# Optimization experiments

Hardware: AMD Instinct MI355X
Metric: run time of the kernel (lower is better)

Reference implementation:

```python
import jax, jax.numpy as jnp
import numpy as np

D = 2048
H = 16
HD = D // H
FF = 4 * D
EPS = 1e-5


def layernorm(x, scale, shift):
    mean = jnp.mean(x, axis=-1, keepdims=True)
    var = jnp.mean((x - mean) ** 2, axis=-1, keepdims=True)  # unbiased=False
    return scale * (x - mean) / jnp.sqrt(var + EPS) + shift


def setup_inputs() -> dict:
    key = jax.random.key(0)
    ks = jax.random.split(key, 12)
    s = 0.02
    return {
        "x": jax.random.normal(ks[0], (2, 2048, D), dtype=jnp.float32),
        "ln1_scale": jnp.ones((D,), jnp.float32),
        "ln1_shift": jnp.zeros((D,), jnp.float32),
        "wq": jax.random.normal(ks[1], (D, D), jnp.float32) * s,
        "bq": jnp.zeros((D,), jnp.float32),
        "wk": jax.random.normal(ks[2], (D, D), jnp.float32) * s,
        "bk": jnp.zeros((D,), jnp.float32),
        "wv": jax.random.normal(ks[3], (D, D), jnp.float32) * s,
        "bv": jnp.zeros((D,), jnp.float32),
        "wo": jax.random.normal(ks[4], (D, D), jnp.float32) * s,
        "bo": jnp.zeros((D,), jnp.float32),
        "ln2_scale": jnp.ones((D,), jnp.float32),
        "ln2_shift": jnp.zeros((D,), jnp.float32),
        "w1": jax.random.normal(ks[5], (D, FF), jnp.float32) * s,
        "b1": jnp.zeros((FF,), jnp.float32),
        "w2": jax.random.normal(ks[6], (FF, D), jnp.float32) * s,
        "b2": jnp.zeros((D,), jnp.float32),
    }


def block(x, ln1_scale, ln1_shift, wq, bq, wk, bk, wv, bv, wo, bo,
          ln2_scale, ln2_shift, w1, b1, w2, b2):
    B, S, _ = x.shape
    h = layernorm(x, ln1_scale, ln1_shift)
    q = (h @ wq + bq).reshape(B, S, H, HD).transpose(0, 2, 1, 3)  # [B,H,S,hd]
    k = (h @ wk + bk).reshape(B, S, H, HD).transpose(0, 2, 1, 3)
    v = (h @ wv + bv).reshape(B, S, H, HD).transpose(0, 2, 1, 3)
    scores = jnp.einsum("bhqd,bhkd->bhqk", q, k) / jnp.sqrt(jnp.float32(HD))
    causal = jnp.tril(jnp.ones((S, S), dtype=bool))
    scores = jnp.where(causal[None, None], scores, -jnp.inf)
    attn = jax.nn.softmax(scores, axis=-1)
    ctx = jnp.einsum("bhqk,bhkd->bhqd", attn, v)
    ctx = ctx.transpose(0, 2, 1, 3).reshape(B, S, D)
    x = x + (ctx @ wo + bo)
    h2 = layernorm(x, ln2_scale, ln2_shift)
    ffn = jax.nn.gelu(h2 @ w1 + b1, approximate=False) @ w2 + b2
    return x + ffn


def reference(x, ln1_scale, ln1_shift, wq, bq, wk, bk, wv, bv, wo, bo,
              ln2_scale, ln2_shift, w1, b1, w2, b2):
    return block(x, ln1_scale, ln1_shift, wq, bq, wk, bk, wv, bv, wo, bo,
                 ln2_scale, ln2_shift, w1, b1, w2, b2)
```

## Files before the change

kernel.cpp:

```cpp
#include <hip/hip_runtime.h>
#include <hip/hip_bf16.h>
#include <math.h>

namespace {

constexpr int Dm  = 2048;
constexpr int FFm = 8192;
constexpr int SEQ = 2048;
constexpr int HDm = 128;
constexpr int MR  = 4096;
constexpr int QW  = 3 * Dm;

typedef __bf16 bf16_t;
typedef __bf16 bf16x8 __attribute__((ext_vector_type(8)));
typedef float  f32x4  __attribute__((ext_vector_type(4)));

typedef __attribute__((address_space(1))) const void as1_void;
typedef __attribute__((address_space(3))) void as3_void;

__device__ __forceinline__ void gload_lds16(const void* g, void* l) {
  __builtin_amdgcn_global_load_lds((as1_void*)g, (as3_void*)l, 16, 0, 0);
}

__global__ __launch_bounds__(256)
void ln_kernel(const float* __restrict__ x, const float* __restrict__ sc,
               const float* __restrict__ sh, bf16_t* __restrict__ out)
{
  const int row = blockIdx.x;
  const int tid = threadIdx.x;
  const float4* xr = (const float4*)(x + (size_t)row * Dm);
  float4 v0 = xr[tid*2], v1 = xr[tid*2+1];
  float s  = v0.x+v0.y+v0.z+v0.w + v1.x+v1.y+v1.z+v1.w;
  float s2 = v0.x*v0.x+v0.y*v0.y+v0.z*v0.z+v0.w*v0.w
           + v1.x*v1.x+v1.y*v1.y+v1.z*v1.z+v1.w*v1.w;
  #pragma unroll
  for (int off = 32; off; off >>= 1) { s += __shfl_xor(s, off); s2 += __shfl_xor(s2, off); }
  __shared__ float red[8];
  if ((tid & 63) == 0) { red[(tid>>6)*2] = s; red[(tid>>6)*2+1] = s2; }
  __syncthreads();
  s  = red[0]+red[2]+red[4]+red[6];
  s2 = red[1]+red[3]+red[5]+red[7];
  const float mean = s * (1.f/Dm);
  const float var  = fmaxf(s2 * (1.f/Dm) - mean*mean, 0.f);
  const float rstd = rsqrtf(var + 1e-5f);
  const float4* scp = (const float4*)sc;
  const float4* shp = (const float4*)sh;
  float4 sc0 = scp[tid*2], sc1 = scp[tid*2+1];
  float4 sh0 = shp[tid*2], sh1 = shp[tid*2+1];
  __attribute__((aligned(16))) bf16_t ob[8];
  ob[0] = (bf16_t)((v0.x-mean)*rstd*sc0.x + sh0.x);
  ob[1] = (bf16_t)((v0.y-mean)*rstd*sc0.y + sh0.y);
  ob[2] = (bf16_t)((v0.z-mean)*rstd*sc0.z + sh0.z);
  ob[3] = (bf16_t)((v0.w-mean)*rstd*sc0.w + sh0.w);
  ob[4] = (bf16_t)((v1.x-mean)*rstd*sc1.x + sh1.x);
  ob[5] = (bf16_t)((v1.y-mean)*rstd*sc1.y + sh1.y);
  ob[6] = (bf16_t)((v1.z-mean)*rstd*sc1.z + sh1.z);
  ob[7] = (bf16_t)((v1.w-mean)*rstd*sc1.w + sh1.w);
  *(uint4*)(out + (size_t)row*Dm + tid*8) = *(const uint4*)ob;
}

__global__ __launch_bounds__(256)
void wconv_t(const float* __restrict__ W, bf16_t* __restrict__ WT, int K, int N)
{
  __shared__ float tile[32][33];
  const int tx = threadIdx.x & 31, ty = threadIdx.x >> 5;
  const int nb = blockIdx.x * 32, kb = blockIdx.y * 32;
  #pragma unroll
  for (int p = 0; p < 4; ++p)
    tile[ty+8*p][tx] = W[(size_t)(kb+ty+8*p)*N + nb + tx];
  __syncthreads();
  #pragma unroll
  for (int p = 0; p < 4; ++p)
    WT[(size_t)(nb+ty+8*p)*K + kb + tx] = (bf16_t)tile[tx][ty+8*p];
}

__global__ void bias_concat(const float* __restrict__ bq, const float* __restrict__ bk,
                            const float* __restrict__ bv, float* __restrict__ o)
{
  int i = blockIdx.x*256 + threadIdx.x;
  o[i] = bq[i]; o[Dm+i] = bk[i]; o[2*Dm+i] = bv[i];
}

__global__ __launch_bounds__(256)
void vtrans(const bf16_t* __restrict__ qkv, bf16_t* __restrict__ vT)
{
  __shared__ bf16_t tile[32][33];
  const int tx = threadIdx.x & 31, ty = threadIdx.x >> 5;
  const int s0 = blockIdx.x*32, d0 = blockIdx.y*32, bh = blockIdx.z;
  const int b = bh >> 4, h = bh & 15;
  const bf16_t* src = qkv + (size_t)(b*SEQ)*QW + 2*Dm + h*HDm;
  #pragma unroll
  for (int p = 0; p < 4; ++p)
    tile[ty+8*p][tx] = src[(size_t)(s0+ty+8*p)*QW + d0 + tx];
  __syncthreads();
  bf16_t* dst = vT + (size_t)bh*HDm*SEQ;
  #pragma unroll
  for (int p = 0; p < 4; ++p)
    dst[(size_t)(d0+ty+8*p)*SEQ + s0 + tx] = tile[tx][ty+8*p];
}

template<int MODE>
__global__ __launch_bounds__(512, 2)
void gemm8p(const bf16_t* __restrict__ A, const bf16_t* __restrict__ BT,
            const float* __restrict__ bias, const float* __restrict__ resid,
            void* __restrict__ Cout, void* __restrict__ Cout2,
            int Ndim, int Kslice, int Kstride, int gx)
{
  const int nwg = gridDim.x;
  int flat = blockIdx.x;
  flat = (flat & 7) * (nwg >> 3) + (flat >> 3);
  const int n0 = (flat % gx) * 256;
  const int m0 = (flat / gx) * 256;
  const int kOff = blockIdx.y * Kslice;
  const int tid = threadIdx.x;
  const int lane = tid & 63;
  const int w = tid >> 6;
  const int wr = w >> 2, wc = w & 3;
  const int lr = lane & 15, kg = lane >> 4;

  __shared__ __attribute__((aligned(16))) bf16_t lds[65536];

  f32x4 acc[8][4] = {};

  auto stageA = [&](int buf, int half, int kt) {
    const bf16_t* src = A + (size_t)(m0 + half*128)*Kstride + kOff + kt*64;
    bf16_t* dst = lds + ((buf*2+0)*2+half)*8192;
    #pragma unroll
    for (int i = 0; i < 2; ++i) {
      const int s = tid + i*512;
      const int row = s >> 3, blk = (s & 7) ^ (row & 7);
      gload_lds16(src + (size_t)row*Kstride + blk*8, dst + s*8);
    }
  };
  auto stageB = [&](int buf, int half, int kt) {
    const bf16_t* src = BT + (size_t)(n0 + half*128)*Kstride + kOff + kt*64;
    bf16_t* dst = lds + ((buf*2+1)*2+half)*8192;
    #pragma unroll
    for (int i = 0; i < 2; ++i) {
      const int s = tid + i*512;
      const int row = s >> 3, blk = (s & 7) ^ (row & 7);
      gload_lds16(src + (size_t)row*Kstride + blk*8, dst + s*8);
    }
  };
  auto readA = [&](int buf, int mh, bf16x8* f) {
    const bf16_t* base = lds + ((buf*2+0)*2+wr)*8192;
    #pragma unroll
    for (int ml = 0; ml < 4; ++ml)
      #pragma unroll
      for (int kk = 0; kk < 2; ++kk) {
        const int row = mh*64 + ml*16 + lr;
        f[ml*2+kk] = *(const bf16x8*)(base + row*64 + (((kk*4+kg) ^ (row&7))*8));
      }
  };
  auto readB = [&](int buf, int nh, bf16x8* f) {
    const bf16_t* base = lds + ((buf*2+1)*2+(wc>>1))*8192;
    #pragma unroll
    for (int nl = 0; nl < 2; ++nl)
      #pragma unroll
      for (int kk = 0; kk < 2; ++kk) {
        const int row = (wc&1)*64 + nh*32 + nl*16 + lr;
        f[nl*2+kk] = *(const bf16x8*)(base + row*64 + (((kk*4+kg) ^ (row&7))*8));
      }
  };
  auto mfma16 = [&](int mh, int nh, const bf16x8* Af, const bf16x8* Bf) {
    __builtin_amdgcn_s_setprio(1);
    #pragma unroll
    for (int ml = 0; ml < 4; ++ml)
      #pragma unroll
      for (int nl = 0; nl < 2; ++nl)
        #pragma unroll
        for (int kk = 0; kk < 2; ++kk)
          acc[mh*4+ml][nh*2+nl] =
            __builtin_amdgcn_mfma_f32_16x16x32_bf16(Af[ml*2+kk], Bf[nl*2+kk],
                                                    acc[mh*4+ml][nh*2+nl], 0, 0, 0);
    __builtin_amdgcn_s_setprio(0);
  };

#define PHASE_MID() do { __builtin_amdgcn_s_barrier(); \
    asm volatile("s_waitcnt lgkmcnt(0)" ::: "memory"); \
    __builtin_amdgcn_sched_barrier(0); } while (0)
#define PHASE_END() __builtin_amdgcn_s_barrier()
#define KGUARD(more_) do { if (more_) asm volatile("s_waitcnt vmcnt(4)" ::: "memory"); \
    else asm volatile("s_waitcnt vmcnt(0)" ::: "memory"); \
    __builtin_amdgcn_s_barrier(); } while (0)

  stageA(0,0,0); stageA(0,1,0); stageB(0,0,0); stageB(0,1,0);
  stageA(1,0,1); stageA(1,1,1);
  asm volatile("s_waitcnt vmcnt(4)" ::: "memory");
  __builtin_amdgcn_s_barrier();

  const int NITER = Kslice >> 7;
  for (int j = 0; j < NITER; ++j) {
    const int t0 = 2*j, t1 = 2*j + 1;
    const bool more = (j + 1 < NITER);
    bf16x8 Af0[8], Af1[8], Bf0[4], Bf1[4];

    readA(0,0,Af0); readB(0,0,Bf0);
    stageB(1,0,t1);
    PHASE_MID(); mfma16(0,0,Af0,Bf0); PHASE_END();
    readA(0,1,Af1);
    stageB(1,1,t1);
    PHASE_MID(); mfma16(1,0,Af1,Bf0); PHASE_END();
    readB(0,1,Bf1);
    if (more) stageA(0,0,t0+2);
    PHASE_MID(); mfma16(1,1,Af1,Bf1); PHASE_END();
    if (more) stageA(0,1,t0+2);
    PHASE_MID(); mfma16(0,1,Af0,Bf1);
    KGUARD(more);

    readA(1,0,Af0); readB(1,0,Bf0);
    if (more) stageB(0,0,t0+2);
    PHASE_MID(); mfma16(0,0,Af0,Bf0); PHASE_END();
    readA(1,1,Af1);
    if (more) stageB(0,1,t0+2);
    PHASE_MID(); mfma16(1,0,Af1,Bf0); PHASE_END();
    readB(1,1,Bf1);
    if (more) stageA(1,0,t1+2);
    PHASE_MID(); mfma16(1,1,Af1,Bf1); PHASE_END();
    if (more) stageA(1,1,t1+2);
    PHASE_MID(); mfma16(0,1,Af0,Bf1);
    KGUARD(more);
  }
#undef PHASE_MID
#undef PHASE_END
#undef KGUARD

  const int cr0 = m0 + wr*128 + kg*4;
  float* pout = nullptr;
  if constexpr (MODE == 3) pout = (float*)(blockIdx.y ? Cout2 : Cout);
  #pragma unroll
  for (int nf = 0; nf < 4; ++nf) {
    const int col = n0 + wc*64 + nf*16 + lr;
    float bv = 0.f;
    if constexpr (MODE != 3) bv = bias[col];
    #pragma unroll
    for (int mf = 0; mf < 8; ++mf) {
      const int rbase = cr0 + mf*16;
      #pragma unroll
      for (int jj = 0; jj < 4; ++jj) {
        float v = acc[mf][nf][jj] + bv;
        const size_t idx = (size_t)(rbase + jj)*Ndim + col;
        if constexpr (MODE == 1) v = 0.5f*v*(1.f + erff(v*0.70710678118f));
        if constexpr (MODE == 2) v += resid[idx];
        if constexpr (MODE == 0 || MODE == 1) ((bf16_t*)Cout)[idx] = (bf16_t)v;
        else if constexpr (MODE == 2) ((float*)Cout)[idx] = v;
        else pout[idx] = v;
      }
    }
  }
}

__global__ __launch_bounds__(256)
void splitk_reduce(const float* __restrict__ p0, const float* __restrict__ p1,
                   const float* __restrict__ bias, const float* __restrict__ resid,
                   float* __restrict__ out, int Ndim)
{
  const size_t e = ((size_t)blockIdx.x*256 + threadIdx.x) * 4;
  float4 a = *(const float4*)(p0 + e);
  float4 b = *(const float4*)(p1 + e);
  float4 r = *(const float4*)(resid + e);
  float4 bv = *(const float4*)(bias + (int)(e & (size_t)(Ndim - 1)));
  float4 o;
  o.x = a.x + b.x + bv.x + r.x;
  o.y = a.y + b.y + bv.y + r.y;
  o.z = a.z + b.z + bv.z + r.z;
  o.w = a.w + b.w + bv.w + r.w;
  *(float4*)(out + e) = o;
}

__global__ __launch_bounds__(512, 2)
void flash_attn3(const bf16_t* __restrict__ qkv, const bf16_t* __restrict__ vT,
                 bf16_t* __restrict__ ctx)
{
  const int bid = blockIdx.x;
  const int bh  = (bid & 7) + 8 * ((bid >> 3) & 3);
  const int qi  = 7 - (bid >> 5);
  const int b = bh >> 4, h = bh & 15;
  const int Q0 = qi * 256;
  const int tid = threadIdx.x;
  const int lane = tid & 63;
  const int w = tid >> 6;
  const int lr = lane & 15, kg = lane >> 4;
  const int q0w = Q0 + w * 32;

  __shared__ __attribute__((aligned(16))) bf16_t Ks[64*128];
  __shared__ __attribute__((aligned(16))) bf16_t Vs[128*64];
  __shared__ __attribute__((aligned(16))) bf16_t Plds[8*2048];

  const bf16_t* kbase = qkv + (size_t)(b*SEQ)*QW + Dm + h*HDm;
  const bf16_t* vbase = vT + (size_t)bh*HDm*SEQ;

  bf16x8 qf[2][4];
  #pragma unroll
  for (int rt = 0; rt < 2; ++rt) {
    const bf16_t* qb = qkv + (size_t)(b*SEQ + q0w + rt*16 + lr)*QW + h*HDm;
    #pragma unroll
    for (int g = 0; g < 4; ++g)
      qf[rt][g] = *(const bf16x8*)(qb + g*32 + kg*8);
  }

  const float scl = 0.08838834764831845f * 1.44269504089f;
  float mrow[2][4], lsum[2][4];
  f32x4 oacc[2][8];
  #pragma unroll
  for (int rt = 0; rt < 2; ++rt) {
    #pragma unroll
    for (int j = 0; j < 4; ++j) { mrow[rt][j] = -INFINITY; lsum[rt][j] = 0.f; }
    #pragma unroll
    for (int dt = 0; dt < 8; ++dt) oacc[rt][dt] = (f32x4){0.f,0.f,0.f,0.f};
  }

  auto stage = [&](int k0) {
    #pragma unroll
    for (int i = 0; i < 2; ++i) {
      const int s = tid + i*512;
      const int row = s >> 4, sl = s & 15;
      gload_lds16(kbase + (size_t)(k0 + row)*QW + (sl ^ (row & 7))*8, Ks + s*8);
    }
    #pragma unroll
    for (int i = 0; i < 2; ++i) {
      const int s = tid + i*512;
      const int row = s >> 3, sl = s & 7;
      gload_lds16(vbase + (size_t)row*SEQ + k0 + (sl ^ (row & 7))*8, Vs + s*8);
    }
  };

  const int nsteps = (Q0 + 256) >> 6;
  stage(0);
  for (int t = 0; t < nsteps; ++t) {
    const int k0 = t * 64;
    __syncthreads();
    if (k0 < q0w + 32) {
      f32x4 sa[2][4];
      #pragma unroll
      for (int rt = 0; rt < 2; ++rt)
        #pragma unroll
        for (int ct = 0; ct < 4; ++ct) sa[rt][ct] = (f32x4){0.f,0.f,0.f,0.f};
      #pragma unroll
      for (int ct = 0; ct < 4; ++ct) {
        const int krow = ct*16 + lr;
        #pragma unroll
        for (int g = 0; g < 4; ++g) {
          bf16x8 kf = *(const bf16x8*)(Ks + krow*128 + ((4*g + kg) ^ (krow & 7))*8);
          sa[0][ct] = __builtin_amdgcn_mfma_f32_16x16x32_bf16(qf[0][g], kf, sa[0][ct], 0, 0, 0);
          sa[1][ct] = __builtin_amdgcn_mfma_f32_16x16x32_bf16(qf[1][g], kf, sa[1][ct], 0, 0, 0);
        }
      }
      #pragma unroll
      for (int rt = 0; rt < 2; ++rt)
        #pragma unroll
        for (int ct = 0; ct < 4; ++ct)
          #pragma unroll
          for (int j = 0; j < 4; ++j) sa[rt][ct][j] *= scl;
      if (k0 + 63 > q0w) {
        #pragma unroll
        for (int ct = 0; ct < 4; ++ct) {
          const int kidx = k0 + ct*16 + lr;
          #pragma unroll
          for (int rt = 0; rt < 2; ++rt)
            #pragma unroll
            for (int j = 0; j < 4; ++j) {
              const int qidx = q0w + rt*16 + kg*4 + j;
              if (kidx > qidx) sa[rt][ct][j] = -INFINITY;
            }
        }
      }
      #pragma unroll
      for (int rt = 0; rt < 2; ++rt) {
        #pragma unroll
        for (int j = 0; j < 4; ++j) {
          const int prow = kg*4 + j;
          float x0 = sa[rt][0][j], x1 = sa[rt][1][j], x2 = sa[rt][2][j], x3 = sa[rt][3][j];
          float v = fmaxf(fmaxf(x0, x1), fmaxf(x2, x3));
          v = fmaxf(v, __shfl_xor(v, 1));
          v = fmaxf(v, __shfl_xor(v, 2));
          v = fmaxf(v, __shfl_xor(v, 4));
          v = fmaxf(v, __shfl_xor(v, 8));
          const float mn = fmaxf(mrow[rt][j], v);
          const float alpha = exp2f(mrow[rt][j] - mn);
          mrow[rt][j] = mn;
          float p0 = exp2f(x0 - mn), p1 = exp2f(x1 - mn);
          float p2 = exp2f(x2 - mn), p3 = exp2f(x3 - mn);
          float ss = (p0 + p1) + (p2 + p3);
          ss += __shfl_xor(ss, 1);
          ss += __shfl_xor(ss, 2);
          ss += __shfl_xor(ss, 4);
          ss += __shfl_xor(ss, 8);
          lsum[rt][j] = lsum[rt][j]*alpha + ss;
          #pragma unroll
          for (int dt = 0; dt < 8; ++dt) oacc[rt][dt][j] *= alpha;
          const int base = w*2048 + rt*1024 + prow*64;
          const int sw = (prow & 7) << 3;
          Plds[(base + ( 0 + lr)) ^ sw] = (bf16_t)p0;
          Plds[(base + (16 + lr)) ^ sw] = (bf16_t)p1;
          Plds[(base + (32 + lr)) ^ sw] = (bf16_t)p2;
          Plds[(base + (48 + lr)) ^ sw] = (bf16_t)p3;
        }
      }
      bf16x8 pf[2][2];
      {
        const int sw = (lr & 7) << 3;
        #pragma unroll
        for (int rt = 0; rt < 2; ++rt) {
          pf[rt][0] = *(const bf16x8*)(Plds + ((w*2048 + rt*1024 + lr*64 +      kg*8) ^ sw));
          pf[rt][1] = *(const bf16x8*)(Plds + ((w*2048 + rt*1024 + lr*64 + 32 + kg*8) ^ sw));
        }
      }
      #pragma unroll
      for (int dt = 0; dt < 8; ++dt) {
        const int vrow = dt*16 + lr;
        #pragma unroll
        for (int kc = 0; kc < 2; ++kc) {
          bf16x8 vf = *(const bf16x8*)(Vs + vrow*64 + ((4*kc + kg) ^ (vrow & 7))*8);
          oacc[0][dt] = __builtin_amdgcn_mfma_f32_16x16x32_bf16(pf[0][kc], vf, oacc[0][dt], 0, 0, 0);
          oacc[1][dt] = __builtin_amdgcn_mfma_f32_16x16x32_bf16(pf[1][kc], vf, oacc[1][dt], 0, 0, 0);
        }
      }
    }
    __syncthreads();
    if (t + 1 < nsteps) stage((t + 1) * 64);
  }

  #pragma unroll
  for (int rt = 0; rt < 2; ++rt) {
    bf16_t* cb = ctx + (size_t)(b*SEQ + q0w + rt*16 + kg*4)*Dm + h*HDm;
    #pragma unroll
    for (int j = 0; j < 4; ++j) {
      const float inv = 1.f / lsum[rt][j];
      #pragma unroll
      for (int dt = 0; dt < 8; ++dt)
        cb[(size_t)j*Dm + dt*16 + lr] = (bf16_t)(oacc[rt][dt][j] * inv);
    }
  }
}

}

extern "C" void kernel_launch(void* const* d_in, const int* in_sizes, int n_in,
                              void* d_out, int out_size, void* d_ws, size_t ws_size,
                              hipStream_t stream)
{
  const float* x   = (const float*)d_in[0];
  const float* g1  = (const float*)d_in[1];
  const float* s1  = (const float*)d_in[2];
  const float* wq  = (const float*)d_in[3];
  const float* bq  = (const float*)d_in[4];
  const float* wk  = (const float*)d_in[5];
  const float* bk  = (const float*)d_in[6];
  const float* wv  = (const float*)d_in[7];
  const float* bv  = (const float*)d_in[8];
  const float* wo  = (const float*)d_in[9];
  const float* bo  = (const float*)d_in[10];
  const float* g2  = (const float*)d_in[11];
  const float* s2  = (const float*)d_in[12];
  const float* w1  = (const float*)d_in[13];
  const float* b1  = (const float*)d_in[14];
  const float* w2  = (const float*)d_in[15];
  const float* b2  = (const float*)d_in[16];
  float* out = (float*)d_out;

  char* p = (char*)d_ws;
  bf16_t* wqkvT = (bf16_t*)p;  p += (size_t)QW*Dm*2;
  bf16_t* woT   = (bf16_t*)p;  p += (size_t)Dm*Dm*2;
  bf16_t* w1T   = (bf16_t*)p;  p += (size_t)FFm*Dm*2;
  bf16_t* w2T   = (bf16_t*)p;  p += (size_t)Dm*FFm*2;
  float*  bqkv  = (float*)p;   p += (size_t)QW*4;
  bf16_t* hbuf  = (bf16_t*)p;  p += (size_t)MR*Dm*2;
  bf16_t* qkv   = (bf16_t*)p;  p += (size_t)MR*QW*2;
  bf16_t* vTb   = (bf16_t*)p;  p += (size_t)32*HDm*SEQ*2;
  bf16_t* ctx   = (bf16_t*)p;  p += (size_t)MR*Dm*2;
  float*  x1    = (float*)p;   p += (size_t)MR*Dm*4;
  bf16_t* ffn1  = qkv;
  float*  part0 = (float*)vTb;
  float*  part1 = (float*)wqkvT;

  wconv_t<<<dim3(Dm/32, Dm/32), 256, 0, stream>>>(wq, wqkvT, Dm, Dm);
  wconv_t<<<dim3(Dm/32, Dm/32), 256, 0, stream>>>(wk, wqkvT + (size_t)Dm*Dm, Dm, Dm);
  wconv_t<<<dim3(Dm/32, Dm/32), 256, 0, stream>>>(wv, wqkvT + (size_t)2*Dm*Dm, Dm, Dm);
  wconv_t<<<dim3(Dm/32, Dm/32), 256, 0, stream>>>(wo, woT, Dm, Dm);
  wconv_t<<<dim3(FFm/32, Dm/32), 256, 0, stream>>>(w1, w1T, Dm, FFm);
  wconv_t<<<dim3(Dm/32, FFm/32), 256, 0, stream>>>(w2, w2T, FFm, Dm);
  bias_concat<<<dim3(Dm/256), 256, 0, stream>>>(bq, bk, bv, bqkv);

  ln_kernel<<<dim3(MR), 256, 0, stream>>>(x, g1, s1, hbuf);
  gemm8p<0><<<dim3((QW/256)*(MR/256), 1), 512, 0, stream>>>(
      hbuf, wqkvT, bqkv, nullptr, qkv, nullptr, QW, Dm, Dm, QW/256);
  vtrans<<<dim3(SEQ/32, HDm/32, 32), 256, 0, stream>>>(qkv, vTb);
  flash_attn3<<<dim3(256), 512, 0, stream>>>(qkv, vTb, ctx);
  gemm8p<2><<<dim3((Dm/256)*(MR/256), 1), 512, 0, stream>>>(
      ctx, woT, bo, x, x1, nullptr, Dm, Dm, Dm, Dm/256);
  ln_kernel<<<dim3(MR), 256, 0, stream>>>(x1, g2, s2, hbuf);
  gemm8p<1><<<dim3((FFm/256)*(MR/256), 1), 512, 0, stream>>>(
      hbuf, w1T, b1, nullptr, ffn1, nullptr, FFm, Dm, Dm, FFm/256);
  gemm8p<3><<<dim3((Dm/256)*(MR/256), 2), 512, 0, stream>>>(
      ffn1, w2T, nullptr, nullptr, part0, part1, Dm, FFm/2, FFm, Dm/256);
  splitk_reduce<<<dim3(MR*Dm/1024), 256, 0, stream>>>(part0, part1, b2, x1, out, Dm);
}
```

Measured before the change: 747.5 us.

## Split-K the output projection, remap GEMM tiles into chiplet-grouped blocks, fuse weight conversions

The output-projection GEMM now runs as a 2-way split-K. It writes partial sums into reused workspace, and a reduce kernel adds bias and residual, so the grid has 256 workgroups instead of 128. The GEMM workgroup-to-tile mapping now gives each of the 8 XCD-interleaved block groups a contiguous 2x4 region of the M/N tile grid, aimed at better L2 reuse per chiplet. Global-to-LDS staging now uses precomputed per-thread pointers that advance by a fixed offset, replacing per-call address recomputation. The four DxD weight transposes are merged into one launch. In exchange, the projection pays extra fp32 partial-sum traffic and one more reduce launch.

```diff
diff --git a/kernel.cpp b/kernel.cpp
--- a/kernel.cpp
+++ b/kernel.cpp
@@ -60,6 +60,26 @@
 }
 
 __global__ __launch_bounds__(256)
+void wconv4(const float* __restrict__ wq, const float* __restrict__ wk,
+            const float* __restrict__ wv, const float* __restrict__ wo,
+            bf16_t* __restrict__ dst)
+{
+  const int z = blockIdx.z;
+  const float* W = (z == 0) ? wq : (z == 1) ? wk : (z == 2) ? wv : wo;
+  bf16_t* WT = dst + (size_t)z * Dm * Dm;
+  __shared__ float tile[32][33];
+  const int tx = threadIdx.x & 31, ty = threadIdx.x >> 5;
+  const int nb = blockIdx.x * 32, kb = blockIdx.y * 32;
+  #pragma unroll
+  for (int p = 0; p < 4; ++p)
+    tile[ty+8*p][tx] = W[(size_t)(kb+ty+8*p)*Dm + nb + tx];
+  __syncthreads();
+  #pragma unroll
+  for (int p = 0; p < 4; ++p)
+    WT[(size_t)(nb+ty+8*p)*Dm + kb + tx] = (bf16_t)tile[tx][ty+8*p];
+}
+
+__global__ __launch_bounds__(256)
 void wconv_t(const float* __restrict__ W, bf16_t* __restrict__ WT, int K, int N)
 {
   __shared__ float tile[32][33];
@@ -102,15 +122,17 @@
 template<int MODE>
 __global__ __launch_bounds__(512, 2)
 void gemm8p(const bf16_t* __restrict__ A, const bf16_t* __restrict__ BT,
-            const float* __restrict__ bias, const float* __restrict__ resid,
+            const float* __restrict__ bias,
             void* __restrict__ Cout, void* __restrict__ Cout2,
-            int Ndim, int Kslice, int Kstride, int gx)
-{
-  const int nwg = gridDim.x;
-  int flat = blockIdx.x;
-  flat = (flat & 7) * (nwg >> 3) + (flat >> 3);
-  const int n0 = (flat % gx) * 256;
-  const int m0 = (flat / gx) * 256;
+            int Ndim, int Kslice, int Kstride, int gn)
+{
+  const int gm = (int)gridDim.x / gn;
+  const int cm = gm >> 1, cn = gn >> 2;
+  const int c = blockIdx.x & 7;
+  const int idx = blockIdx.x >> 3;
+  const int mi = idx / cn, ni = idx - mi*cn;
+  const int m0 = ((c >> 2)*cm + mi) * 256;
+  const int n0 = ((c & 3)*cn + ni) * 256;
   const int kOff = blockIdx.y * Kslice;
   const int tid = threadIdx.x;
   const int lane = tid & 63;
@@ -122,28 +144,22 @@
 
   f32x4 acc[8][4] = {};
 
-  auto stageA = [&](int buf, int half, int kt) {
-    const bf16_t* src = A + (size_t)(m0 + half*128)*Kstride + kOff + kt*64;
-    bf16_t* dst = lds + ((buf*2+0)*2+half)*8192;
-    #pragma unroll
-    for (int i = 0; i < 2; ++i) {
-      const int s = tid + i*512;
-      const int row = s >> 3, blk = (s & 7) ^ (row & 7);
-      gload_lds16(src + (size_t)row*Kstride + blk*8, dst + s*8);
-    }
-  };
-  auto stageB = [&](int buf, int half, int kt) {
-    const bf16_t* src = BT + (size_t)(n0 + half*128)*Kstride + kOff + kt*64;
-    bf16_t* dst = lds + ((buf*2+1)*2+half)*8192;
-    #pragma unroll
-    for (int i = 0; i < 2; ++i) {
-      const int s = tid + i*512;
-      const int row = s >> 3, blk = (s & 7) ^ (row & 7);
-      gload_lds16(src + (size_t)row*Kstride + blk*8, dst + s*8);
-    }
-  };
+  const int r1   = tid >> 3;
+  const int blk1 = (tid & 7) ^ (r1 & 7);
+  const size_t rowoff = (size_t)64 * Kstride;
+  const bf16_t* pA0 = A  + (size_t)(m0 + r1)*Kstride       + kOff + blk1*8;
+  const bf16_t* pA1 = A  + (size_t)(m0 + 128 + r1)*Kstride + kOff + blk1*8;
+  const bf16_t* pB0 = BT + (size_t)(n0 + r1)*Kstride       + kOff + blk1*8;
+  const bf16_t* pB1 = BT + (size_t)(n0 + 128 + r1)*Kstride + kOff + blk1*8;
+  bf16_t* const d0 = lds + (size_t)tid*8;
+
+#define STG(p, region) do { \
+    gload_lds16((p), d0 + (region)*8192); \
+    gload_lds16((p) + rowoff, d0 + (region)*8192 + 4096); \
+    (p) += 64; } while (0)
+
   auto readA = [&](int buf, int mh, bf16x8* f) {
-    const bf16_t* base = lds + ((buf*2+0)*2+wr)*8192;
+    const bf16_t* base = lds + (buf*4 + wr)*8192;
     #pragma unroll
     for (int ml = 0; ml < 4; ++ml)
       #pragma unroll
@@ -153,7 +169,7 @@
       }
   };
   auto readB = [&](int buf, int nh, bf16x8* f) {
-    const bf16_t* base = lds + ((buf*2+1)*2+(wc>>1))*8192;
+    const bf16_t* base = lds + (buf*4 + 2 + (wc>>1))*8192;
     #pragma unroll
     for (int nl = 0; nl < 2; ++nl)
       #pragma unroll
@@ -184,46 +200,46 @@
     else asm volatile("s_waitcnt vmcnt(0)" ::: "memory"); \
     __builtin_amdgcn_s_barrier(); } while (0)
 
-  stageA(0,0,0); stageA(0,1,0); stageB(0,0,0); stageB(0,1,0);
-  stageA(1,0,1); stageA(1,1,1);
+  STG(pA0, 0); STG(pA1, 1); STG(pB0, 2); STG(pB1, 3);
+  STG(pA0, 4); STG(pA1, 5);
   asm volatile("s_waitcnt vmcnt(4)" ::: "memory");
   __builtin_amdgcn_s_barrier();
 
   const int NITER = Kslice >> 7;
   for (int j = 0; j < NITER; ++j) {
-    const int t0 = 2*j, t1 = 2*j + 1;
     const bool more = (j + 1 < NITER);
     bf16x8 Af0[8], Af1[8], Bf0[4], Bf1[4];
 
     readA(0,0,Af0); readB(0,0,Bf0);
-    stageB(1,0,t1);
+    STG(pB0, 6);
     PHASE_MID(); mfma16(0,0,Af0,Bf0); PHASE_END();
     readA(0,1,Af1);
-    stageB(1,1,t1);
+    STG(pB1, 7);
     PHASE_MID(); mfma16(1,0,Af1,Bf0); PHASE_END();
     readB(0,1,Bf1);
-    if (more) stageA(0,0,t0+2);
+    if (more) STG(pA0, 0);
     PHASE_MID(); mfma16(1,1,Af1,Bf1); PHASE_END();
-    if (more) stageA(0,1,t0+2);
+    if (more) STG(pA1, 1);
     PHASE_MID(); mfma16(0,1,Af0,Bf1);
     KGUARD(more);
 
     readA(1,0,Af0); readB(1,0,Bf0);
-    if (more) stageB(0,0,t0+2);
+    if (more) STG(pB0, 2);
     PHASE_MID(); mfma16(0,0,Af0,Bf0); PHASE_END();
     readA(1,1,Af1);
-    if (more) stageB(0,1,t0+2);
+    if (more) STG(pB1, 3);
     PHASE_MID(); mfma16(1,0,Af1,Bf0); PHASE_END();
     readB(1,1,Bf1);
-    if (more) stageA(1,0,t1+2);
+    if (more) STG(pA0, 4);
     PHASE_MID(); mfma16(1,1,Af1,Bf1); PHASE_END();
-    if (more) stageA(1,1,t1+2);
+    if (more) STG(pA1, 5);
     PHASE_MID(); mfma16(0,1,Af0,Bf1);
     KGUARD(more);
   }
 #undef PHASE_MID
 #undef PHASE_END
 #undef KGUARD
+#undef STG
 
   const int cr0 = m0 + wr*128 + kg*4;
   float* pout = nullptr;
@@ -241,9 +257,7 @@
         float v = acc[mf][nf][jj] + bv;
         const size_t idx = (size_t)(rbase + jj)*Ndim + col;
         if constexpr (MODE == 1) v = 0.5f*v*(1.f + erff(v*0.70710678118f));
-        if constexpr (MODE == 2) v += resid[idx];
         if constexpr (MODE == 0 || MODE == 1) ((bf16_t*)Cout)[idx] = (bf16_t)v;
-        else if constexpr (MODE == 2) ((float*)Cout)[idx] = v;
         else pout[idx] = v;
       }
     }
@@ -471,28 +485,28 @@
   bf16_t* ctx   = (bf16_t*)p;  p += (size_t)MR*Dm*2;
   float*  x1    = (float*)p;   p += (size_t)MR*Dm*4;
   bf16_t* ffn1  = qkv;
-  float*  part0 = (float*)vTb;
-  float*  part1 = (float*)wqkvT;
-
-  wconv_t<<<dim3(Dm/32, Dm/32), 256, 0, stream>>>(wq, wqkvT, Dm, Dm);
-  wconv_t<<<dim3(Dm/32, Dm/32), 256, 0, stream>>>(wk, wqkvT + (size_t)Dm*Dm, Dm, Dm);
-  wconv_t<<<dim3(Dm/32, Dm/32), 256, 0, stream>>>(wv, wqkvT + (size_t)2*Dm*Dm, Dm, Dm);
-  wconv_t<<<dim3(Dm/32, Dm/32), 256, 0, stream>>>(wo, woT, Dm, Dm);
+  float*  prj0  = (float*)qkv;
+  float*  prj1  = (float*)qkv + (size_t)MR*Dm;
+  float*  f2p0  = (float*)w1T;
+  float*  f2p1  = (float*)wqkvT;
+
+  wconv4<<<dim3(Dm/32, Dm/32, 4), 256, 0, stream>>>(wq, wk, wv, wo, wqkvT);
   wconv_t<<<dim3(FFm/32, Dm/32), 256, 0, stream>>>(w1, w1T, Dm, FFm);
   wconv_t<<<dim3(Dm/32, FFm/32), 256, 0, stream>>>(w2, w2T, FFm, Dm);
   bias_concat<<<dim3(Dm/256), 256, 0, stream>>>(bq, bk, bv, bqkv);
 
   ln_kernel<<<dim3(MR), 256, 0, stream>>>(x, g1, s1, hbuf);
   gemm8p<0><<<dim3((QW/256)*(MR/256), 1), 512, 0, stream>>>(
-      hbuf, wqkvT, bqkv, nullptr, qkv, nullptr, QW, Dm, Dm, QW/256);
+      hbuf, wqkvT, bqkv, qkv, nullptr, QW, Dm, Dm, QW/256);
   vtrans<<<dim3(SEQ/32, HDm/32, 32), 256, 0, stream>>>(qkv, vTb);
   flash_attn3<<<dim3(256), 512, 0, stream>>>(qkv, vTb, ctx);
-  gemm8p<2><<<dim3((Dm/256)*(MR/256), 1), 512, 0, stream>>>(
-      ctx, woT, bo, x, x1, nullptr, Dm, Dm, Dm, Dm/256);
+  gemm8p<3><<<dim3((Dm/256)*(MR/256), 2), 512, 0, stream>>>(
+      ctx, woT, nullptr, prj0, prj1, Dm, Dm/2, Dm, Dm/256);
+  splitk_reduce<<<dim3(MR*Dm/1024), 256, 0, stream>>>(prj0, prj1, bo, x, x1, Dm);
   ln_kernel<<<dim3(MR), 256, 0, stream>>>(x1, g2, s2, hbuf);
   gemm8p<1><<<dim3((FFm/256)*(MR/256), 1), 512, 0, stream>>>(
-      hbuf, w1T, b1, nullptr, ffn1, nullptr, FFm, Dm, Dm, FFm/256);
+      hbuf, w1T, b1, ffn1, nullptr, FFm, Dm, Dm, FFm/256);
   gemm8p<3><<<dim3((Dm/256)*(MR/256), 2), 512, 0, stream>>>(
-      ffn1, w2T, nullptr, nullptr, part0, part1, Dm, FFm/2, FFm, Dm/256);
-  splitk_reduce<<<dim3(MR*Dm/1024), 256, 0, stream>>>(part0, part1, b2, x1, out, Dm);
-}
+      ffn1, w2T, nullptr, f2p0, f2p1, Dm, FFm/2, FFm, Dm/256);
+  splitk_reduce<<<dim3(MR*Dm/1024), 256, 0, stream>>>(f2p0, f2p1, b2, x1, out, Dm);
+}
```

Measured after the change: 724.1 us. -3.1%, faster.
